# Kernel tuning notes

Hardware: AMD Instinct MI355X
Metric: run time of the kernel (lower is better)

The kernel has to match this reference:

```python
import jax, jax.numpy as jnp
import numpy as np

B, C, H, W = 2, 256, 64, 64
KEEP = 0.1


def setup_inputs() -> dict:
    key = jax.random.key(0)
    ks = jax.random.split(key, 7)
    s = 0.05  # small init for 1x1-conv weights
    return {
        "x": jax.random.normal(ks[0], (B, C, H, W), dtype=jnp.float32),
        "Wq": jax.random.normal(ks[1], (C, C), dtype=jnp.float32) * s,
        "bq": jax.random.normal(ks[2], (C,), dtype=jnp.float32) * s,
        "Wk": jax.random.normal(ks[3], (C, C), dtype=jnp.float32) * s,
        "bk": jax.random.normal(ks[4], (C,), dtype=jnp.float32) * s,
        "Wv": jax.random.normal(ks[5], (C, C), dtype=jnp.float32) * s,
        "bv": jax.random.normal(ks[6], (C,), dtype=jnp.float32) * s,
    }


def reference(x, Wq, bq, Wk, bk, Wv, bv):
    b, c, h, w = x.shape
    n = h * w

    def proj(Wm, bm):
        # 1x1 conv == per-pixel linear; output as [B, N, C] tokens
        return jnp.einsum('bchw,oc->bhwo', x, Wm).reshape(b, n, c) + bm

    q = proj(Wq, bq)
    k = proj(Wk, bk)
    v = proj(Wv, bv)

    scores = jnp.einsum('bnc,bmc->bnm', q, k) / (c ** 0.5)  # [B, N, N]
    k_keep = max(1, int(KEEP * n))

    vals, idx = jax.lax.top_k(scores, k_keep)  # [B, N, k_keep]
    # softmax over -inf-masked scores == softmax over topk vals scattered into zeros
    probs = jax.nn.softmax(vals, axis=-1)
    attn = jnp.zeros_like(scores).at[
        jnp.arange(b)[:, None, None], jnp.arange(n)[None, :, None], idx
    ].set(probs)

    out = jnp.einsum('bnm,bmc->bnc', attn, v)  # [B, N, C]
    return out.transpose(0, 2, 1).reshape(b, c, h, w)
```

## Files before the change

kernel.cpp:

```cpp
#include <hip/hip_runtime.h>
#include <hip/hip_bf16.h>
#include <math.h>

#define BATCH 2
#define CC    256
#define NN    4096
#define KK    409
#define KCAT  768
#define SCALE 0.0625f
#define PSTRIDE 4096

typedef _Float16 half8 __attribute__((ext_vector_type(8)));
typedef unsigned short ushort8 __attribute__((ext_vector_type(8)));
typedef float    floatx4 __attribute__((ext_vector_type(4)));

typedef __attribute__((address_space(3))) unsigned       lds_u32;
typedef __attribute__((address_space(1))) const unsigned glb_u32;
__device__ __forceinline__ void gload16(const void* g, void* l) {
    __builtin_amdgcn_global_load_lds((glb_u32*)g, (lds_u32*)l, 16, 0, 0);
}

__global__ __launch_bounds__(256) void xpose_wcat_kernel(
        const float* __restrict__ x,
        const float* __restrict__ Wq, const float* __restrict__ Wk,
        const float* __restrict__ Wv,
        _Float16* __restrict__ xcat, _Float16* __restrict__ Wcat) {
    const int t  = threadIdx.x;
    if (blockIdx.y == 4) {
        int idx = (blockIdx.z * 64 + blockIdx.x) * 256 + t;
#pragma unroll
        for (int k = 0; k < 6; k++) {
            int e = idx + k * 32768;
            int mat = e >> 16;
            int o   = (e >> 8) & 255;
            int c   = e & 255;
            const float* W = (mat == 0) ? Wq : (mat == 1) ? Wk : Wv;
            float v = W[o * 256 + c];
            _Float16 hi = (_Float16)v;
            _Float16 lo = (_Float16)(v - (float)hi);
            _Float16* wr = Wcat + ((size_t)(mat * 256 + o)) * KCAT;
            wr[c] = hi; wr[256 + c] = hi; wr[512 + c] = lo;
        }
        return;
    }

    __shared__ float xs[64][68];
    const int n0 = blockIdx.x * 64;
    const int c0 = blockIdx.y * 64;
    const int b  = blockIdx.z;

    {
        const int ci = t >> 2;
        const int j  = (t & 3) * 16;
        const float* xp = x + ((size_t)((b << 8) + c0 + ci)) * NN + n0 + j;
        float4 a0 = ((const float4*)xp)[0];
        float4 a1 = ((const float4*)xp)[1];
        float4 a2 = ((const float4*)xp)[2];
        float4 a3 = ((const float4*)xp)[3];
        *(float4*)&xs[ci][j]      = a0;
        *(float4*)&xs[ci][j + 4]  = a1;
        *(float4*)&xs[ci][j + 8]  = a2;
        *(float4*)&xs[ci][j + 12] = a3;
    }
    __syncthreads();

    const int n = t >> 2;
    const int g0 = t & 3;
    _Float16* xr = xcat + ((size_t)(b * NN + n0 + n)) * KCAT + c0;
#pragma unroll
    for (int gg = 0; gg < 2; gg++) {
        int g = g0 + gg * 4;
        half8 hi, lo;
#pragma unroll
        for (int k = 0; k < 8; k++) {
            float v = xs[g * 8 + k][n];
            _Float16 h = (_Float16)v;
            hi[k] = h;
            lo[k] = (_Float16)(v - (float)h);
        }
        *(half8*)(xr + g * 8)       = hi;
        *(half8*)(xr + 256 + g * 8) = lo;
        *(half8*)(xr + 512 + g * 8) = hi;
    }
}

__global__ __launch_bounds__(256) void proj_gemm(
        const _Float16* __restrict__ xcat, const _Float16* __restrict__ Wcat,
        const float* __restrict__ bq, const float* __restrict__ bk,
        const float* __restrict__ bv,
        _Float16* __restrict__ Qcat, _Float16* __restrict__ Kcat,
        _Float16* __restrict__ Vt) {
    __shared__ _Float16 As[2][128][64];
    __shared__ _Float16 Bs[2][128][64];

    const int t    = threadIdx.x;
    const int wave = t >> 6;
    const int l    = t & 63;
    const int wr   = wave >> 1;
    const int wc   = wave & 1;
    const int mat  = blockIdx.z;

    int bym, bxn;
    if (mat < 2) { bym = blockIdx.x >> 1; bxn = blockIdx.x & 1; }
    else         { bym = blockIdx.x & 1;  bxn = blockIdx.x >> 1; }

    const int lr = l >> 3;
    const int gg = (l & 7) ^ lr;

    const _Float16* At;
    const _Float16* Bt;
    if (mat < 2) {
        At = xcat + ((size_t)(bym * 128)) * KCAT;
        Bt = Wcat + ((size_t)(mat * 256 + bxn * 128)) * KCAT;
    } else {
        At = Wcat + ((size_t)(512 + bym * 128)) * KCAT;
        Bt = xcat + ((size_t)(bxn * 128)) * KCAT;
    }
    const size_t lane_off = (size_t)lr * KCAT + gg * 8;

    floatx4 acc[4][4];
#pragma unroll
    for (int i = 0; i < 4; i++)
#pragma unroll
        for (int j = 0; j < 4; j++) acc[i][j] = (floatx4)0.0f;

    const int rowA = l & 15;
    const int sg0  = (l >> 4) ^ (l & 7);
    const int sg1  = sg0 ^ 4;

#pragma unroll
    for (int s = 0; s < 4; s++) {
        const int seg = wave * 4 + s;
        gload16(At + (size_t)seg * 8 * KCAT + lane_off, &As[0][seg * 8][0]);
        gload16(Bt + (size_t)seg * 8 * KCAT + lane_off, &Bs[0][seg * 8][0]);
    }
    __syncthreads();

    for (int kt = 0; kt < 12; ++kt) {
        const int cur = kt & 1;
        if (kt < 11) {
            const int kc = (kt + 1) * 64;
#pragma unroll
            for (int s = 0; s < 4; s++) {
                const int seg = wave * 4 + s;
                gload16(At + (size_t)seg * 8 * KCAT + lane_off + kc,
                        &As[cur ^ 1][seg * 8][0]);
                gload16(Bt + (size_t)seg * 8 * KCAT + lane_off + kc,
                        &Bs[cur ^ 1][seg * 8][0]);
            }
        }
#pragma unroll
        for (int ks = 0; ks < 2; ks++) {
            const int sg = ks ? sg1 : sg0;
            half8 af[4], bf[4];
#pragma unroll
            for (int mi = 0; mi < 4; mi++)
                af[mi] = *(const half8*)&As[cur][wr * 64 + mi * 16 + rowA][sg * 8];
#pragma unroll
            for (int ni = 0; ni < 4; ni++)
                bf[ni] = *(const half8*)&Bs[cur][wc * 64 + ni * 16 + rowA][sg * 8];
#pragma unroll
            for (int mi = 0; mi < 4; mi++)
#pragma unroll
                for (int ni = 0; ni < 4; ni++)
                    acc[mi][ni] = __builtin_amdgcn_mfma_f32_16x16x32_f16(
                        af[mi], bf[ni], acc[mi][ni], 0, 0, 0);
        }
        __syncthreads();
    }

    if (mat < 2) {
        const float* bias = (mat == 0) ? bq : bk;
        _Float16* Out = (mat == 0) ? Qcat : Kcat;
#pragma unroll
        for (int ni = 0; ni < 4; ni++) {
            int ch = bxn * 128 + wc * 64 + ni * 16 + (l & 15);
            float bb = bias[ch];
#pragma unroll
            for (int mi = 0; mi < 4; mi++)
#pragma unroll
                for (int rg = 0; rg < 4; rg++) {
                    int token = bym * 128 + wr * 64 + mi * 16 + (l >> 4) * 4 + rg;
                    float v = acc[mi][ni][rg] + bb;
                    _Float16 hi = (_Float16)v;
                    _Float16 lo = (_Float16)(v - (float)hi);
                    _Float16* p = Out + (size_t)token * KCAT + ch;
                    if (mat == 0) { p[0] = hi; p[256] = lo; p[512] = hi; }
                    else          { p[0] = hi; p[256] = hi; p[512] = lo; }
                }
        }
    } else {
#pragma unroll
        for (int mi = 0; mi < 4; mi++)
#pragma unroll
            for (int rg = 0; rg < 4; rg++) {
                int ch = bym * 128 + wr * 64 + mi * 16 + (l >> 4) * 4 + rg;
                float bb = bv[ch];
#pragma unroll
                for (int ni = 0; ni < 4; ni++) {
                    int col = bxn * 128 + wc * 64 + ni * 16 + (l & 15);
                    int b = col >> 12, n = col & 4095;
                    Vt[((size_t)((b << 8) + ch)) * NN + n] =
                        (_Float16)(acc[mi][ni][rg] + bb);
                }
            }
    }
}

__global__ __launch_bounds__(512, 2) void score_gemm(
        const _Float16* __restrict__ Qcat, const _Float16* __restrict__ Kcat,
        _Float16* __restrict__ S) {
    __shared__ _Float16 As[2][256][64];
    __shared__ _Float16 Bs[2][256][64];

    const int t    = threadIdx.x;
    const int wave = t >> 6;
    const int l    = t & 63;
    const int wr   = wave >> 1;
    const int wc   = wave & 1;

    const int id  = blockIdx.x;
    const int sc  = id & 7;
    const int j   = id >> 3;
    const int b   = sc & 1;
    const int scq = sc >> 1;
    const int bxn = ((scq & 1) << 3) + (j & 7);
    const int bym = ((scq >> 1) << 3) + (j >> 3);

    const int lr = l >> 3;
    const int gg = (l & 7) ^ lr;

    const _Float16* At = Qcat + ((size_t)((b << 12) + bym * 256)) * KCAT;
    const _Float16* Bt = Kcat + ((size_t)((b << 12) + bxn * 256)) * KCAT;
    const size_t lane_off = (size_t)lr * KCAT + gg * 8;

    floatx4 acc[4][8];
#pragma unroll
    for (int i = 0; i < 4; i++)
#pragma unroll
        for (int jj = 0; jj < 8; jj++) acc[i][jj] = (floatx4)0.0f;

    const int rowA = l & 15;
    const int sg0  = (l >> 4) ^ (l & 7);
    const int sg1  = sg0 ^ 4;

#pragma unroll
    for (int s = 0; s < 4; s++) {
        const int seg = wave * 4 + s;
        gload16(At + (size_t)seg * 8 * KCAT + lane_off, &As[0][seg * 8][0]);
        gload16(Bt + (size_t)seg * 8 * KCAT + lane_off, &Bs[0][seg * 8][0]);
    }

    for (int kt = 0; kt < 12; ++kt) {
        const int cur = kt & 1;
        if (kt < 11) {
            const int kc = (kt + 1) * 64;
#pragma unroll
            for (int s = 0; s < 4; s++) {
                const int seg = wave * 4 + s;
                gload16(At + (size_t)seg * 8 * KCAT + lane_off + kc,
                        &As[cur ^ 1][seg * 8][0]);
                gload16(Bt + (size_t)seg * 8 * KCAT + lane_off + kc,
                        &Bs[cur ^ 1][seg * 8][0]);
            }
            asm volatile("s_waitcnt vmcnt(8)" ::: "memory");
        } else {
            asm volatile("s_waitcnt vmcnt(0)" ::: "memory");
        }
        __builtin_amdgcn_s_barrier();
        asm volatile("" ::: "memory");

#pragma unroll
        for (int ks = 0; ks < 2; ks++) {
            const int sg = ks ? sg1 : sg0;
            half8 af[4], bf[8];
#pragma unroll
            for (int mi = 0; mi < 4; mi++)
                af[mi] = *(const half8*)&As[cur][wr * 64 + mi * 16 + rowA][sg * 8];
#pragma unroll
            for (int ni = 0; ni < 8; ni++)
                bf[ni] = *(const half8*)&Bs[cur][wc * 128 + ni * 16 + rowA][sg * 8];
#pragma unroll
            for (int mi = 0; mi < 4; mi++)
#pragma unroll
                for (int ni = 0; ni < 8; ni++)
                    acc[mi][ni] = __builtin_amdgcn_mfma_f32_16x16x32_f16(
                        af[mi], bf[ni], acc[mi][ni], 0, 0, 0);
        }
        __builtin_amdgcn_s_barrier();
        asm volatile("" ::: "memory");
    }

    _Float16* Sb = S + ((size_t)b << 24);
#pragma unroll
    for (int mi = 0; mi < 4; mi++)
#pragma unroll
        for (int ni = 0; ni < 8; ni++) {
            int col = bxn * 256 + wc * 128 + ni * 16 + (l & 15);
#pragma unroll
            for (int rg = 0; rg < 4; rg++) {
                int row = bym * 256 + wr * 64 + mi * 16 + (l >> 4) * 4 + rg;
                Sb[((size_t)row << 12) + col] =
                    (_Float16)(acc[mi][ni][rg] * SCALE);
            }
        }
}

__global__ __launch_bounds__(256) void select_scatter(
        const _Float16* __restrict__ S, _Float16* __restrict__ P) {
    __shared__ unsigned hist[256];
    __shared__ unsigned scan[256];
    __shared__ unsigned candKey[NN];
    __shared__ unsigned wred[4];
    __shared__ float    wsum[4];
    __shared__ unsigned sh_d, sh_cntgt, sh_T;
    __shared__ int      sh_ncand, sh_need;

    const int t = threadIdx.x;
    const int l = t & 63;
    const int w = t >> 6;

    unsigned (*hist4)[256] = (unsigned (*)[256])candKey;

    float          val[16];
    unsigned short ukey[16];
    {
        const unsigned short* Srow =
            (const unsigned short*)(S + ((size_t)blockIdx.x << 12));
        ushort8 u0 = *(const ushort8*)(Srow + t * 16);
        ushort8 u1 = *(const ushort8*)(Srow + t * 16 + 8);
#pragma unroll
        for (int jj = 0; jj < 8; jj++) {
            unsigned short a = u0[jj], b = u1[jj];
            ukey[jj]     = (a & 0x8000u) ? (unsigned short)~a
                                         : (unsigned short)(a | 0x8000u);
            ukey[jj + 8] = (b & 0x8000u) ? (unsigned short)~b
                                         : (unsigned short)(b | 0x8000u);
            _Float16 ha, hb;
            __builtin_memcpy(&ha, &a, 2);
            __builtin_memcpy(&hb, &b, 2);
            val[jj]     = (float)ha;
            val[jj + 8] = (float)hb;
        }
    }

#pragma unroll
    for (int w2 = 0; w2 < 4; w2++) hist4[w2][t] = 0u;
    if (t == 0) sh_ncand = 0;
    __syncthreads();

#pragma unroll
    for (int j = 0; j < 16; j++) atomicAdd(&hist4[w][ukey[j] >> 8], 1u);
    __syncthreads();
    hist[t] = hist4[0][t] + hist4[1][t] + hist4[2][t] + hist4[3][t];

    int rem = KK;

    auto find_digit = [&](int remv) {
        unsigned v = hist[t];
#pragma unroll
        for (int off = 1; off < 64; off <<= 1) {
            unsigned o = __shfl_down(v, off);
            if (l + off < 64) v += o;
        }
        if (l == 0) wred[w] = v;
        __syncthreads();
        unsigned add = 0u;
#pragma unroll
        for (int w2 = 0; w2 < 4; w2++) if (w2 > w) add += wred[w2];
        scan[t] = v + add;
        __syncthreads();
        unsigned sufd  = scan[t];
        unsigned sufd1 = (t < 255) ? scan[t + 1] : 0u;
        if (sufd >= (unsigned)remv && sufd1 < (unsigned)remv) {
            sh_d = (unsigned)t; sh_cntgt = sufd1;
        }
        __syncthreads();
    };

    find_digit(rem);
    const unsigned dbin = sh_d;
    rem -= (int)sh_cntgt;

#pragma unroll
    for (int j = 0; j < 16; j++) {
        if ((unsigned)(ukey[j] >> 8) == dbin) {
            int slot = atomicAdd(&sh_ncand, 1);
            candKey[slot] = ukey[j];
        }
    }
    __syncthreads();
    const int nc = sh_ncand;

    if (nc <= 256) {
        if (t < nc) {
            const unsigned ki = candKey[t];
            int g = 0, m = 0;
            for (int j = 0; j < nc; j++) {
                unsigned kj = candKey[j];
                g += (kj > ki) ? 1 : 0;
                m += (kj == ki) ? 1 : 0;
            }
            if (g < rem && g + m >= rem) {
                sh_T = ki; sh_need = rem - g;
            }
        }
    } else {
        hist[t] = 0u;
        __syncthreads();
        for (int i = t; i < nc; i += 256)
            atomicAdd(&hist[candKey[i] & 255u], 1u);
        __syncthreads();
        find_digit(rem);
        if (t == 0) { sh_T = (dbin << 8) | sh_d; sh_need = rem - (int)sh_cntgt; }
    }
    __syncthreads();
    const unsigned short Tk = (unsigned short)sh_T;
    const int need = sh_need;
    float mT;
    {
        unsigned short tu = (Tk & 0x8000u) ? (unsigned short)(Tk ^ 0x8000u)
                                           : (unsigned short)~Tk;
        _Float16 th;
        __builtin_memcpy(&th, &tu, 2);
        mT = (float)th;
    }

    int eqc = 0;
#pragma unroll
    for (int j = 0; j < 16; j++) if (ukey[j] == Tk) eqc++;
    int vinc = eqc;
#pragma unroll
    for (int off = 1; off < 64; off <<= 1) {
        int o = __shfl_up(vinc, off);
        if (l >= off) vinc += o;
    }
    if (l == 63) wred[w] = (unsigned)vinc;
    __syncthreads();
    int addlow = 0;
#pragma unroll
    for (int w2 = 0; w2 < 4; w2++) if (w2 < w) addlow += (int)wred[w2];
    const int eqexcl = vinc - eqc + addlow;

    float pv[16];
    float le = 0.f;
#pragma unroll
    for (int j = 0; j < 16; j++) {
        float e = 0.f;
        if (ukey[j] > Tk) { e = __expf(val[j] - mT); le += e; }
        pv[j] = e;
    }
    if (eqc) {
        int seen = 0;
#pragma unroll
        for (int j = 0; j < 16; j++) {
            if (ukey[j] == Tk) {
                if (eqexcl + seen < need) { pv[j] = 1.0f; le += 1.0f; }
                seen++;
            }
        }
    }

#pragma unroll
    for (int off = 32; off > 0; off >>= 1) {
        float o = __shfl_down(le, off);
        if (l + off < 64) le += o;
    }
    if (l == 0) wsum[w] = le;
    __syncthreads();
    const float inv = 1.0f / (wsum[0] + wsum[1] + wsum[2] + wsum[3]);

    half8 ra, rb;
#pragma unroll
    for (int j = 0; j < 8; j++) {
        ra[j] = (_Float16)(pv[j] * inv);
        rb[j] = (_Float16)(pv[j + 8] * inv);
    }
    _Float16* Pr = P + (size_t)blockIdx.x * PSTRIDE + t * 16;
    *(half8*)Pr       = ra;
    *(half8*)(Pr + 8) = rb;
}

__global__ __launch_bounds__(256) void av_gemm(
        const _Float16* __restrict__ Vt, const _Float16* __restrict__ P,
        float* __restrict__ out) {
    __shared__ _Float16 As[4][64][64];
    __shared__ _Float16 Bs[4][64][64];

    const int t    = threadIdx.x;
    const int wave = t >> 6;
    const int l    = t & 63;
    const int wr   = wave >> 1;
    const int wc   = wave & 1;
    const int bxn  = blockIdx.x;
    const int byc  = blockIdx.y;
    const int b    = blockIdx.z;

    const int lr = l >> 3;
    const int gg = (l & 7) ^ lr;

    const _Float16* At = Vt + ((size_t)((b << 8) + byc * 64)) * NN;
    const _Float16* Bt = P + ((size_t)(b * NN + bxn * 64)) * PSTRIDE;
    const size_t lane_offA = (size_t)lr * NN + gg * 8;
    const size_t lane_offB = (size_t)lr * PSTRIDE + gg * 8;

    floatx4 acc[2][2];
#pragma unroll
    for (int i = 0; i < 2; i++)
#pragma unroll
        for (int j = 0; j < 2; j++) acc[i][j] = (floatx4)0.0f;

    const int rowA   = l & 15;
    const int sgbase = (l >> 4) ^ (l & 7);

    for (int kt = 0; kt < 16; ++kt) {
        const int kc = kt * 256;
#pragma unroll
        for (int c = 0; c < 4; c++)
#pragma unroll
            for (int s = 0; s < 2; s++) {
                const int seg = wave * 2 + s;
                gload16(At + (size_t)seg * 8 * NN + lane_offA + kc + c * 64,
                        &As[c][seg * 8][0]);
                gload16(Bt + (size_t)seg * 8 * PSTRIDE + lane_offB + kc + c * 64,
                        &Bs[c][seg * 8][0]);
            }
        __syncthreads();
#pragma unroll
        for (int c = 0; c < 4; c++)
#pragma unroll
            for (int st = 0; st < 2; st++) {
                const int sg = sgbase ^ (st ? 4 : 0);
                half8 af[2], bf[2];
#pragma unroll
                for (int mi = 0; mi < 2; mi++)
                    af[mi] = *(const half8*)&As[c][wr * 32 + mi * 16 + rowA][sg * 8];
#pragma unroll
                for (int ni = 0; ni < 2; ni++)
                    bf[ni] = *(const half8*)&Bs[c][wc * 32 + ni * 16 + rowA][sg * 8];
#pragma unroll
                for (int mi = 0; mi < 2; mi++)
#pragma unroll
                    for (int ni = 0; ni < 2; ni++)
                        acc[mi][ni] = __builtin_amdgcn_mfma_f32_16x16x32_f16(
                            af[mi], bf[ni], acc[mi][ni], 0, 0, 0);
            }
        __syncthreads();
    }

#pragma unroll
    for (int mi = 0; mi < 2; mi++)
#pragma unroll
        for (int ni = 0; ni < 2; ni++) {
            int col = bxn * 64 + wc * 32 + ni * 16 + (l & 15);
#pragma unroll
            for (int rg = 0; rg < 4; rg++) {
                int row = byc * 64 + wr * 32 + mi * 16 + (l >> 4) * 4 + rg;
                out[((size_t)((b << 8) + row) << 12) + col] = acc[mi][ni][rg];
            }
        }
}

extern "C" void kernel_launch(void* const* d_in, const int* in_sizes, int n_in,
                              void* d_out, int out_size, void* d_ws, size_t ws_size,
                              hipStream_t stream) {
    const float* x  = (const float*)d_in[0];
    const float* Wq = (const float*)d_in[1];
    const float* bq = (const float*)d_in[2];
    const float* Wk = (const float*)d_in[3];
    const float* bk = (const float*)d_in[4];
    const float* Wv = (const float*)d_in[5];
    const float* bv = (const float*)d_in[6];
    float* out = (float*)d_out;

    char* ws = (char*)d_ws;
    _Float16* Wcat = (_Float16*)ws;
    _Float16* Qcat = (_Float16*)(ws + 1179648);
    _Float16* Kcat = (_Float16*)(ws + 1179648 + 12582912);
    _Float16* Vt   = (_Float16*)(ws + 1179648 + 2 * 12582912);
    _Float16* S    = (_Float16*)(ws + 1179648 + 2 * 12582912 + 4194304);
    _Float16* xcat = (_Float16*)S;
    _Float16* P    = (_Float16*)S;

    xpose_wcat_kernel<<<dim3(64, 5, BATCH), 256, 0, stream>>>(x, Wq, Wk, Wv,
                                                              xcat, Wcat);
    proj_gemm<<<dim3(128, 1, 3), 256, 0, stream>>>(xcat, Wcat, bq, bk, bv,
                                                   Qcat, Kcat, Vt);
    score_gemm<<<dim3(512, 1, 1), 512, 0, stream>>>(Qcat, Kcat, S);
    select_scatter<<<BATCH * NN, 256, 0, stream>>>(S, P);
    av_gemm<<<dim3(64, 4, BATCH), 256, 0, stream>>>(Vt, P, out);
}
```

Baseline: 237.6 us.

## Double-buffer AV GEMM loads and compact top-k candidates via prefix scan

The AV GEMM now keeps two LDS buffers, prefetching the next K-tile with global_load_lds while MFMAs consume the current one, and uses explicit vmcnt waits plus raw barriers in place of __syncthreads. In select_scatter, candidate compaction switches from a shared atomic counter to a wave/block prefix scan, and keys are unpacked from 32-bit words instead of ushort vectors. The goal is to hide global-load latency in the GEMM and avoid LDS atomic contention during selection. Doubling LDS to 64KB per block may reduce occupancy, and the hand-written waitcnt depends on the compiler issuing loads in the expected order.

```diff
diff --git a/kernel.cpp b/kernel.cpp
--- a/kernel.cpp
+++ b/kernel.cpp
@@ -11,7 +11,6 @@
 #define PSTRIDE 4096
 
 typedef _Float16 half8 __attribute__((ext_vector_type(8)));
-typedef unsigned short ushort8 __attribute__((ext_vector_type(8)));
 typedef float    floatx4 __attribute__((ext_vector_type(4)));
 
 typedef __attribute__((address_space(3))) unsigned       lds_u32;
@@ -314,7 +313,7 @@
     __shared__ unsigned wred[4];
     __shared__ float    wsum[4];
     __shared__ unsigned sh_d, sh_cntgt, sh_T;
-    __shared__ int      sh_ncand, sh_need;
+    __shared__ int      sh_need;
 
     const int t = threadIdx.x;
     const int l = t & 63;
@@ -322,31 +321,31 @@
 
     unsigned (*hist4)[256] = (unsigned (*)[256])candKey;
 
-    float          val[16];
-    unsigned short ukey[16];
+    float    val[16];
+    unsigned ukey[16];
     {
-        const unsigned short* Srow =
-            (const unsigned short*)(S + ((size_t)blockIdx.x << 12));
-        ushort8 u0 = *(const ushort8*)(Srow + t * 16);
-        ushort8 u1 = *(const ushort8*)(Srow + t * 16 + 8);
-#pragma unroll
-        for (int jj = 0; jj < 8; jj++) {
-            unsigned short a = u0[jj], b = u1[jj];
-            ukey[jj]     = (a & 0x8000u) ? (unsigned short)~a
-                                         : (unsigned short)(a | 0x8000u);
-            ukey[jj + 8] = (b & 0x8000u) ? (unsigned short)~b
-                                         : (unsigned short)(b | 0x8000u);
-            _Float16 ha, hb;
-            __builtin_memcpy(&ha, &a, 2);
-            __builtin_memcpy(&hb, &b, 2);
-            val[jj]     = (float)ha;
-            val[jj + 8] = (float)hb;
+        const uint4* Srow = (const uint4*)
+            ((const unsigned short*)(S + ((size_t)blockIdx.x << 12)) + t * 16);
+        uint4 d0 = Srow[0];
+        uint4 d1 = Srow[1];
+        unsigned wb[8] = {d0.x, d0.y, d0.z, d0.w, d1.x, d1.y, d1.z, d1.w};
+#pragma unroll
+        for (int p = 0; p < 8; p++) {
+            unsigned lo = wb[p] & 0xFFFFu;
+            unsigned hi = wb[p] >> 16;
+            ukey[2 * p]     = lo ^ ((lo & 0x8000u) ? 0xFFFFu : 0x8000u);
+            ukey[2 * p + 1] = hi ^ ((hi & 0x8000u) ? 0xFFFFu : 0x8000u);
+            unsigned short ls = (unsigned short)lo, hs = (unsigned short)hi;
+            _Float16 lh, hh;
+            __builtin_memcpy(&lh, &ls, 2);
+            __builtin_memcpy(&hh, &hs, 2);
+            val[2 * p]     = (float)lh;
+            val[2 * p + 1] = (float)hh;
         }
     }
 
 #pragma unroll
     for (int w2 = 0; w2 < 4; w2++) hist4[w2][t] = 0u;
-    if (t == 0) sh_ncand = 0;
     __syncthreads();
 
 #pragma unroll
@@ -382,15 +381,26 @@
     const unsigned dbin = sh_d;
     rem -= (int)sh_cntgt;
 
-#pragma unroll
-    for (int j = 0; j < 16; j++) {
-        if ((unsigned)(ukey[j] >> 8) == dbin) {
-            int slot = atomicAdd(&sh_ncand, 1);
-            candKey[slot] = ukey[j];
-        }
-    }
-    __syncthreads();
-    const int nc = sh_ncand;
+    int cnt = 0;
+#pragma unroll
+    for (int j = 0; j < 16; j++) if ((ukey[j] >> 8) == dbin) cnt++;
+    int pre = cnt;
+#pragma unroll
+    for (int off = 1; off < 64; off <<= 1) {
+        int o = __shfl_up(pre, off);
+        if (l >= off) pre += o;
+    }
+    if (l == 63) wred[w] = (unsigned)pre;
+    __syncthreads();
+    int base = 0;
+#pragma unroll
+    for (int w2 = 0; w2 < 4; w2++) if (w2 < w) base += (int)wred[w2];
+    const int nc = (int)(wred[0] + wred[1] + wred[2] + wred[3]);
+    int slot = base + pre - cnt;
+#pragma unroll
+    for (int j = 0; j < 16; j++)
+        if ((ukey[j] >> 8) == dbin) candKey[slot++] = ukey[j];
+    __syncthreads();
 
     if (nc <= 256) {
         if (t < nc) {
@@ -415,14 +425,14 @@
         if (t == 0) { sh_T = (dbin << 8) | sh_d; sh_need = rem - (int)sh_cntgt; }
     }
     __syncthreads();
-    const unsigned short Tk = (unsigned short)sh_T;
+    const unsigned Tk = sh_T;
     const int need = sh_need;
     float mT;
     {
-        unsigned short tu = (Tk & 0x8000u) ? (unsigned short)(Tk ^ 0x8000u)
-                                           : (unsigned short)~Tk;
+        unsigned tu = (Tk & 0x8000u) ? (Tk ^ 0x8000u) : (~Tk & 0xFFFFu);
+        unsigned short ts = (unsigned short)tu;
         _Float16 th;
-        __builtin_memcpy(&th, &tu, 2);
+        __builtin_memcpy(&th, &ts, 2);
         mT = (float)th;
     }
 
@@ -484,8 +494,8 @@
 __global__ __launch_bounds__(256) void av_gemm(
         const _Float16* __restrict__ Vt, const _Float16* __restrict__ P,
         float* __restrict__ out) {
-    __shared__ _Float16 As[4][64][64];
-    __shared__ _Float16 Bs[4][64][64];
+    __shared__ _Float16 As[2][4][64][64];
+    __shared__ _Float16 Bs[2][4][64][64];
 
     const int t    = threadIdx.x;
     const int wave = t >> 6;
@@ -513,19 +523,38 @@
     const int rowA   = l & 15;
     const int sgbase = (l >> 4) ^ (l & 7);
 
+#pragma unroll
+    for (int c = 0; c < 4; c++)
+#pragma unroll
+        for (int s = 0; s < 2; s++) {
+            const int seg = wave * 2 + s;
+            gload16(At + (size_t)seg * 8 * NN + lane_offA + c * 64,
+                    &As[0][c][seg * 8][0]);
+            gload16(Bt + (size_t)seg * 8 * PSTRIDE + lane_offB + c * 64,
+                    &Bs[0][c][seg * 8][0]);
+        }
+
     for (int kt = 0; kt < 16; ++kt) {
-        const int kc = kt * 256;
-#pragma unroll
-        for (int c = 0; c < 4; c++)
-#pragma unroll
-            for (int s = 0; s < 2; s++) {
-                const int seg = wave * 2 + s;
-                gload16(At + (size_t)seg * 8 * NN + lane_offA + kc + c * 64,
-                        &As[c][seg * 8][0]);
-                gload16(Bt + (size_t)seg * 8 * PSTRIDE + lane_offB + kc + c * 64,
-                        &Bs[c][seg * 8][0]);
-            }
-        __syncthreads();
+        const int cur = kt & 1;
+        if (kt < 15) {
+            const int kc = (kt + 1) * 256;
+#pragma unroll
+            for (int c = 0; c < 4; c++)
+#pragma unroll
+                for (int s = 0; s < 2; s++) {
+                    const int seg = wave * 2 + s;
+                    gload16(At + (size_t)seg * 8 * NN + lane_offA + kc + c * 64,
+                            &As[cur ^ 1][c][seg * 8][0]);
+                    gload16(Bt + (size_t)seg * 8 * PSTRIDE + lane_offB + kc + c * 64,
+                            &Bs[cur ^ 1][c][seg * 8][0]);
+                }
+            asm volatile("s_waitcnt vmcnt(16)" ::: "memory");
+        } else {
+            asm volatile("s_waitcnt vmcnt(0)" ::: "memory");
+        }
+        __builtin_amdgcn_s_barrier();
+        asm volatile("" ::: "memory");
+
 #pragma unroll
         for (int c = 0; c < 4; c++)
 #pragma unroll
@@ -534,10 +563,10 @@
                 half8 af[2], bf[2];
 #pragma unroll
                 for (int mi = 0; mi < 2; mi++)
-                    af[mi] = *(const half8*)&As[c][wr * 32 + mi * 16 + rowA][sg * 8];
+                    af[mi] = *(const half8*)&As[cur][c][wr * 32 + mi * 16 + rowA][sg * 8];
 #pragma unroll
                 for (int ni = 0; ni < 2; ni++)
-                    bf[ni] = *(const half8*)&Bs[c][wc * 32 + ni * 16 + rowA][sg * 8];
+                    bf[ni] = *(const half8*)&Bs[cur][c][wc * 32 + ni * 16 + rowA][sg * 8];
 #pragma unroll
                 for (int mi = 0; mi < 2; mi++)
 #pragma unroll
@@ -545,7 +574,8 @@
                         acc[mi][ni] = __builtin_amdgcn_mfma_f32_16x16x32_f16(
                             af[mi], bf[ni], acc[mi][ni], 0, 0, 0);
             }
-        __syncthreads();
+        __builtin_amdgcn_s_barrier();
+        asm volatile("" ::: "memory");
     }
 
 #pragma unroll
```

Result: slower. 251.7 us (+5.9%).

## Pack select keys two per register and compact candidates via prefix scan

Applied to the files above, without the earlier changes.

The top-k select kernel now keeps the order-preserving keys packed two per 32-bit register, with no separate float values. Values are decoded from the keys when needed, and exponentials are recomputed in the output pass rather than held in a 16-float array, which lowers register pressure. Candidate compaction uses a wave and block prefix scan instead of a shared atomic counter, which also gives a deterministic candidate order. The cost is redundant expf and decode work, plus an extra barrier for the scan.

```diff
diff --git a/kernel.cpp b/kernel.cpp
--- a/kernel.cpp
+++ b/kernel.cpp
@@ -11,13 +11,20 @@
 #define PSTRIDE 4096
 
 typedef _Float16 half8 __attribute__((ext_vector_type(8)));
-typedef unsigned short ushort8 __attribute__((ext_vector_type(8)));
 typedef float    floatx4 __attribute__((ext_vector_type(4)));
 
 typedef __attribute__((address_space(3))) unsigned       lds_u32;
 typedef __attribute__((address_space(1))) const unsigned glb_u32;
 __device__ __forceinline__ void gload16(const void* g, void* l) {
     __builtin_amdgcn_global_load_lds((glb_u32*)g, (lds_u32*)l, 16, 0, 0);
+}
+
+__device__ __forceinline__ float keyval(unsigned k) {
+    unsigned tops = (k >> 15) & 1u;
+    unsigned u = k ^ (0x8000u | ((1u - tops) * 0x7FFFu));
+    unsigned short us = (unsigned short)u;
+    _Float16 h; __builtin_memcpy(&h, &us, 2);
+    return (float)h;
 }
 
 __global__ __launch_bounds__(256) void xpose_wcat_kernel(
@@ -314,7 +321,7 @@
     __shared__ unsigned wred[4];
     __shared__ float    wsum[4];
     __shared__ unsigned sh_d, sh_cntgt, sh_T;
-    __shared__ int      sh_ncand, sh_need;
+    __shared__ int      sh_need;
 
     const int t = threadIdx.x;
     const int l = t & 63;
@@ -322,35 +329,32 @@
 
     unsigned (*hist4)[256] = (unsigned (*)[256])candKey;
 
-    float          val[16];
-    unsigned short ukey[16];
+    unsigned kp[8];
     {
-        const unsigned short* Srow =
-            (const unsigned short*)(S + ((size_t)blockIdx.x << 12));
-        ushort8 u0 = *(const ushort8*)(Srow + t * 16);
-        ushort8 u1 = *(const ushort8*)(Srow + t * 16 + 8);
-#pragma unroll
-        for (int jj = 0; jj < 8; jj++) {
-            unsigned short a = u0[jj], b = u1[jj];
-            ukey[jj]     = (a & 0x8000u) ? (unsigned short)~a
-                                         : (unsigned short)(a | 0x8000u);
-            ukey[jj + 8] = (b & 0x8000u) ? (unsigned short)~b
-                                         : (unsigned short)(b | 0x8000u);
-            _Float16 ha, hb;
-            __builtin_memcpy(&ha, &a, 2);
-            __builtin_memcpy(&hb, &b, 2);
-            val[jj]     = (float)ha;
-            val[jj + 8] = (float)hb;
-        }
-    }
+        const uint4* Srow = (const uint4*)
+            ((const unsigned short*)(S + ((size_t)blockIdx.x << 12)) + t * 16);
+        uint4 d0 = Srow[0];
+        uint4 d1 = Srow[1];
+        unsigned wb[8] = {d0.x, d0.y, d0.z, d0.w, d1.x, d1.y, d1.z, d1.w};
+#pragma unroll
+        for (int p = 0; p < 8; p++) {
+            unsigned tops = (wb[p] >> 15) & 0x10001u;
+            kp[p] = wb[p] ^ ((tops * 0xFFFFu) | 0x80008000u);
+        }
+    }
+    auto KEY = [&](int j) -> unsigned {
+        return (j & 1) ? (kp[j >> 1] >> 16) : (kp[j >> 1] & 0xFFFFu);
+    };
 
 #pragma unroll
     for (int w2 = 0; w2 < 4; w2++) hist4[w2][t] = 0u;
-    if (t == 0) sh_ncand = 0;
-    __syncthreads();
-
-#pragma unroll
-    for (int j = 0; j < 16; j++) atomicAdd(&hist4[w][ukey[j] >> 8], 1u);
+    __syncthreads();
+
+#pragma unroll
+    for (int p = 0; p < 8; p++) {
+        atomicAdd(&hist4[w][(kp[p] >> 8) & 255u], 1u);
+        atomicAdd(&hist4[w][kp[p] >> 24], 1u);
+    }
     __syncthreads();
     hist[t] = hist4[0][t] + hist4[1][t] + hist4[2][t] + hist4[3][t];
 
@@ -382,15 +386,28 @@
     const unsigned dbin = sh_d;
     rem -= (int)sh_cntgt;
 
+    int cnt = 0;
+#pragma unroll
+    for (int j = 0; j < 16; j++) if ((KEY(j) >> 8) == dbin) cnt++;
+    int pre = cnt;
+#pragma unroll
+    for (int off = 1; off < 64; off <<= 1) {
+        int o = __shfl_up(pre, off);
+        if (l >= off) pre += o;
+    }
+    if (l == 63) wred[w] = (unsigned)pre;
+    __syncthreads();
+    int base = 0;
+#pragma unroll
+    for (int w2 = 0; w2 < 4; w2++) if (w2 < w) base += (int)wred[w2];
+    const int nc = (int)(wred[0] + wred[1] + wred[2] + wred[3]);
+    int slot = base + pre - cnt;
 #pragma unroll
     for (int j = 0; j < 16; j++) {
-        if ((unsigned)(ukey[j] >> 8) == dbin) {
-            int slot = atomicAdd(&sh_ncand, 1);
-            candKey[slot] = ukey[j];
-        }
-    }
-    __syncthreads();
-    const int nc = sh_ncand;
+        unsigned k = KEY(j);
+        if ((k >> 8) == dbin) candKey[slot++] = k;
+    }
+    __syncthreads();
 
     if (nc <= 256) {
         if (t < nc) {
@@ -415,20 +432,13 @@
         if (t == 0) { sh_T = (dbin << 8) | sh_d; sh_need = rem - (int)sh_cntgt; }
     }
     __syncthreads();
-    const unsigned short Tk = (unsigned short)sh_T;
+    const unsigned Tk = sh_T;
     const int need = sh_need;
-    float mT;
-    {
-        unsigned short tu = (Tk & 0x8000u) ? (unsigned short)(Tk ^ 0x8000u)
-                                           : (unsigned short)~Tk;
-        _Float16 th;
-        __builtin_memcpy(&th, &tu, 2);
-        mT = (float)th;
-    }
+    const float mT = keyval(Tk);
 
     int eqc = 0;
 #pragma unroll
-    for (int j = 0; j < 16; j++) if (ukey[j] == Tk) eqc++;
+    for (int j = 0; j < 16; j++) if (KEY(j) == Tk) eqc++;
     int vinc = eqc;
 #pragma unroll
     for (int off = 1; off < 64; off <<= 1) {
@@ -442,23 +452,17 @@
     for (int w2 = 0; w2 < 4; w2++) if (w2 < w) addlow += (int)wred[w2];
     const int eqexcl = vinc - eqc + addlow;
 
-    float pv[16];
     float le = 0.f;
 #pragma unroll
     for (int j = 0; j < 16; j++) {
-        float e = 0.f;
-        if (ukey[j] > Tk) { e = __expf(val[j] - mT); le += e; }
-        pv[j] = e;
-    }
-    if (eqc) {
-        int seen = 0;
-#pragma unroll
-        for (int j = 0; j < 16; j++) {
-            if (ukey[j] == Tk) {
-                if (eqexcl + seen < need) { pv[j] = 1.0f; le += 1.0f; }
-                seen++;
-            }
-        }
+        unsigned k = KEY(j);
+        if (k > Tk) le += __expf(keyval(k) - mT);
+    }
+    {
+        int nsel = need - eqexcl;
+        if (nsel < 0) nsel = 0;
+        if (nsel > eqc) nsel = eqc;
+        for (int i = 0; i < nsel; i++) le += 1.0f;
     }
 
 #pragma unroll
@@ -471,10 +475,21 @@
     const float inv = 1.0f / (wsum[0] + wsum[1] + wsum[2] + wsum[3]);
 
     half8 ra, rb;
-#pragma unroll
-    for (int j = 0; j < 8; j++) {
-        ra[j] = (_Float16)(pv[j] * inv);
-        rb[j] = (_Float16)(pv[j + 8] * inv);
+    {
+        int seen = 0;
+#pragma unroll
+        for (int j = 0; j < 16; j++) {
+            unsigned k = KEY(j);
+            float e = 0.f;
+            if (k > Tk) {
+                e = __expf(keyval(k) - mT) * inv;
+            } else if (k == Tk) {
+                if (eqexcl + seen < need) e = inv;
+                seen++;
+            }
+            if (j < 8) ra[j] = (_Float16)e;
+            else       rb[j - 8] = (_Float16)e;
+        }
     }
     _Float16* Pr = P + (size_t)blockIdx.x * PSTRIDE + t * 16;
     *(half8*)Pr       = ra;
```

Result: slower. 242.7 us (+2.1%).
